# Kernel tuning notes

Hardware: AMD Instinct MI355X
Metric: run time of the kernel (lower is better)

Reference implementation:

```python
import jax, jax.numpy as jnp
import numpy as np

B, N, IN, OUT, H, F = 4, 2048, 128, 64, 4, 64


def setup_inputs() -> dict:
    key = jax.random.key(0)
    ks = jax.random.split(key, 10)
    h = jax.random.normal(ks[0], (B, N, IN), dtype=jnp.float32)
    projection_matrix = jax.random.uniform(ks[1], (B, N, N), dtype=jnp.float32)
    similarity_matrix = jnp.tanh(jax.random.normal(ks[2], (B, N, N), dtype=jnp.float32))
    quadrant_matrix = jax.random.randint(ks[3], (B, N, N, 2), 0, 4)
    # learned params (xavier-ish scaling); stored as (in, out) so x @ W
    W = jax.random.normal(ks[4], (IN, OUT * H), dtype=jnp.float32) * (1.0 / np.sqrt(IN))
    random_projection = jax.random.normal(ks[5], (IN, F), dtype=jnp.float32) * 0.1
    a_q = jax.random.normal(ks[6], (2 * F, OUT), dtype=jnp.float32) * (1.0 / np.sqrt(2 * F))
    a_k = jax.random.normal(ks[7], (2 * F, OUT), dtype=jnp.float32) * (1.0 / np.sqrt(2 * F))
    quadrant_bias = jax.random.normal(ks[8], (4, 4), dtype=jnp.float32) * 0.02
    output_proj = jax.random.normal(ks[9], (OUT * H, OUT), dtype=jnp.float32) * (1.0 / np.sqrt(OUT * H))
    return {
        "h": h,
        "projection_matrix": projection_matrix,
        "similarity_matrix": similarity_matrix,
        "W": W,
        "random_projection": random_projection,
        "a_q": a_q,
        "a_k": a_k,
        "quadrant_bias": quadrant_bias,
        "output_proj": output_proj,
        "quadrant_matrix": quadrant_matrix,
    }


def reference(h, projection_matrix, similarity_matrix, W, random_projection,
              a_q, a_k, quadrant_bias, output_proj, quadrant_matrix):
    # random feature map: phi = [cos(h R), sin(h R)]  -> (B, N, 2F)
    proj = jnp.einsum('bnd,df->bnf', h, random_projection)
    phi = jnp.concatenate([jnp.cos(proj), jnp.sin(proj)], axis=-1)
    Q = phi @ a_q                       # (B, N, OUT)
    K = phi @ a_k                       # (B, N, OUT)
    Wh = (h @ W).reshape(h.shape[0], h.shape[1], H, OUT)  # (B, N, H, OUT)

    scores = jnp.einsum('bio,bjo->bij', Q, K)             # (B, N, N)
    # additive relational biases (shared across heads)
    qb = quadrant_bias[quadrant_matrix[..., 0], quadrant_matrix[..., 1]]  # (B, N, N)
    scores = scores + projection_matrix + similarity_matrix + qb
    attn = jax.nn.softmax(scores[:, None, :, :], axis=-1)  # (B, H, N, N) via broadcast

    # aggregate values per head, then concat heads
    hp = jnp.einsum('bhij,bjhk->bihk', attn, Wh)           # (B, N, H, OUT)
    hp = hp.reshape(h.shape[0], h.shape[1], H * OUT)
    out = hp @ output_proj                                  # (B, N, OUT)
    return jax.nn.elu(out)
```

## Files before the change

### kernel.cpp

```cpp
#include <hip/hip_runtime.h>
#include <math.h>

#define BB   4
#define NN   2048
#define IND  128
#define CDIM 256
#define NIT  16

typedef _Float16 half_t;
typedef _Float16 half4_t __attribute__((ext_vector_type(4)));
typedef _Float16 half8_t __attribute__((ext_vector_type(8)));
typedef float    f32x4   __attribute__((ext_vector_type(4)));

#define SHIFT 16.0f
#define BSCL  6.103515625e-05f
#define BOFF  (-17.5f)

#define NPRE  (BB * NN / 8)
#define NFUSE 2048

__global__ __launch_bounds__(256) void pre_fuse_kernel(
    const float* __restrict__ hg,
    const float* __restrict__ W,
    const float* __restrict__ R,
    const float* __restrict__ aq,
    const float* __restrict__ ak,
    const float* __restrict__ pm,
    const float* __restrict__ sm,
    const int*   __restrict__ qm,
    const float* __restrict__ qbias,
    half_t* __restrict__ Qw,
    half_t* __restrict__ Kw,
    half_t* __restrict__ WhJ,
    unsigned short* __restrict__ bf)
{
    const int tid = threadIdx.x;

    __shared__ float hs[8][IND];
    __shared__ float phis[8][IND];
    __shared__ float qbs[16];

    if (blockIdx.x >= NPRE) {
        if (tid < 16) qbs[tid] = qbias[tid];
        __syncthreads();
        const int nquad  = BB * NN * NN / 4;
        const int stride = NFUSE * 256;
        for (int idx = (blockIdx.x - NPRE) * 256 + tid; idx < nquad; idx += stride) {
            const float4 p  = ((const float4*)pm)[idx];
            const float4 s  = ((const float4*)sm)[idx];
            const int4   qa = ((const int4*)qm)[(size_t)idx * 2];
            const int4   qb = ((const int4*)qm)[(size_t)idx * 2 + 1];
            const float f0 = p.x + s.x + qbs[(qa.x << 2) | qa.y];
            const float f1 = p.y + s.y + qbs[(qa.z << 2) | qa.w];
            const float f2 = p.z + s.z + qbs[(qb.x << 2) | qb.y];
            const float f3 = p.w + s.w + qbs[(qb.z << 2) | qb.w];
            const unsigned u0 = __float2uint_rn(fminf(fmaxf((f0 + 1.5f) * 16384.f, 0.f), 65535.f));
            const unsigned u1 = __float2uint_rn(fminf(fmaxf((f1 + 1.5f) * 16384.f, 0.f), 65535.f));
            const unsigned u2 = __float2uint_rn(fminf(fmaxf((f2 + 1.5f) * 16384.f, 0.f), 65535.f));
            const unsigned u3 = __float2uint_rn(fminf(fmaxf((f3 + 1.5f) * 16384.f, 0.f), 65535.f));
            uint2 o; o.x = u0 | (u1 << 16); o.y = u2 | (u3 << 16);
            ((uint2*)bf)[idx] = o;
        }
        return;
    }

    const int row0 = blockIdx.x * 8;

    {
        const float4* src = (const float4*)(hg + (size_t)row0 * IND);
        ((float4*)&hs[0][0])[tid] = src[tid];
    }
    __syncthreads();

    {
        const int f  = tid & 63;
        const int rr = tid >> 6;
        float p0 = 0.f, p1 = 0.f;
        #pragma unroll 4
        for (int d0 = 0; d0 < IND; d0 += 4) {
            const float r0 = R[(d0 + 0) * 64 + f];
            const float r1 = R[(d0 + 1) * 64 + f];
            const float r2 = R[(d0 + 2) * 64 + f];
            const float r3 = R[(d0 + 3) * 64 + f];
            const float4 ha = *(const float4*)&hs[rr][d0];
            const float4 hb = *(const float4*)&hs[rr + 4][d0];
            p0 += ha.x * r0 + ha.y * r1 + ha.z * r2 + ha.w * r3;
            p1 += hb.x * r0 + hb.y * r1 + hb.z * r2 + hb.w * r3;
        }
        float s, c;
        __sincosf(p0, &s, &c); phis[rr][f]     = c; phis[rr][f + 64]     = s;
        __sincosf(p1, &s, &c); phis[rr + 4][f] = c; phis[rr + 4][f + 64] = s;
    }

    {
        float acc[8];
        #pragma unroll
        for (int r = 0; r < 8; ++r) acc[r] = 0.f;
        #pragma unroll 2
        for (int d0 = 0; d0 < IND; d0 += 4) {
            const float w0 = W[(d0 + 0) * CDIM + tid];
            const float w1 = W[(d0 + 1) * CDIM + tid];
            const float w2 = W[(d0 + 2) * CDIM + tid];
            const float w3 = W[(d0 + 3) * CDIM + tid];
            #pragma unroll
            for (int r = 0; r < 8; ++r) {
                const float4 h4 = *(const float4*)&hs[r][d0];
                acc[r] += h4.x * w0 + h4.y * w1 + h4.z * w2 + h4.w * w3;
            }
        }
        const int b   = row0 >> 11;
        const int j16 = (row0 & (NN - 1)) >> 4;
        const int jr0 = row0 & 8;
        half8_t v;
        #pragma unroll
        for (int r = 0; r < 8; ++r) v[r] = (half_t)acc[r];
        *(half8_t*)(WhJ + (((size_t)b * 128 + j16) * CDIM + tid) * 16 + jr0) = v;
    }
    __syncthreads();

    {
        const int o  = tid & 63;
        const int qk = (tid >> 6) & 1;
        const int rh = tid >> 7;
        const float* A = qk ? ak : aq;
        half_t*    Dst = qk ? Kw : Qw;
        float acc[4] = {0.f, 0.f, 0.f, 0.f};
        #pragma unroll 2
        for (int t0 = 0; t0 < IND; t0 += 4) {
            const float a0 = A[(t0 + 0) * 64 + o];
            const float a1 = A[(t0 + 1) * 64 + o];
            const float a2 = A[(t0 + 2) * 64 + o];
            const float a3 = A[(t0 + 3) * 64 + o];
            #pragma unroll
            for (int r = 0; r < 4; ++r) {
                const float4 ph = *(const float4*)&phis[rh * 4 + r][t0];
                acc[r] += ph.x * a0 + ph.y * a1 + ph.z * a2 + ph.w * a3;
            }
        }
        #pragma unroll
        for (int r = 0; r < 4; ++r)
            Dst[(size_t)(row0 + rh * 4 + r) * 64 + o] = (half_t)acc[r];
    }
}

#define ITERS(IT, KC0, KC1, KN0, KN1, UB, PB)                                   \
  {                                                                             \
       \
    const half_t* wpt = wb + (size_t)(IT) * (8 * CDIM * 16);                    \
    half4_t bwv[16];                                                            \
    _Pragma("unroll")                                                           \
    for (int kk = 0; kk < 8; ++kk) {                                            \
      bwv[2 * kk]     = *(const half4_t*)(wpt + (size_t)kk * (CDIM * 16));      \
      bwv[2 * kk + 1] = *(const half4_t*)(wpt + (size_t)kk * (CDIM * 16) + 256);\
    }                                                                           \
                                     \
    f32x4 s4 = (f32x4){0.f, 0.f, 0.f, 0.f};                                     \
    s4 = __builtin_amdgcn_mfma_f32_16x16x32_f16(KC0, qf0, s4, 0, 0, 0);         \
    s4 = __builtin_amdgcn_mfma_f32_16x16x32_f16(KC1, qf1, s4, 0, 0, 0);         \
    if ((IT) + 1 < NIT) {                                                       \
      const half_t* kp = kbase + (size_t)((IT) + 1) * 128 * 64;                 \
      KN0 = *(const half8_t*)(kp + q * 8);                                      \
      KN1 = *(const half8_t*)(kp + 32 + q * 8);                                 \
    }                                                                           \
    const uint2 uc = UB;                                                        \
    if ((IT) + 2 < NIT)                                                         \
      UB = *(const uint2*)(bfr + (size_t)((IT) + 2) * 128 + cbase);             \
    const float sv0 = s4[0] + fmaf((float)(uc.x & 0xffffu), BSCL, BOFF);        \
    const float sv1 = s4[1] + fmaf((float)(uc.x >> 16),     BSCL, BOFF);        \
    const float sv2 = s4[2] + fmaf((float)(uc.y & 0xffffu), BSCL, BOFF);        \
    const float sv3 = s4[3] + fmaf((float)(uc.y >> 16),     BSCL, BOFF);        \
    const half_t h0 = (half_t)__expf(fminf(sv0, 11.f));                         \
    const half_t h1 = (half_t)__expf(fminf(sv1, 11.f));                         \
    const half_t h2 = (half_t)__expf(fminf(sv2, 11.f));                         \
    const half_t h3 = (half_t)__expf(fminf(sv3, 11.f));                         \
    half4_t aP; aP[0] = h0; aP[1] = h1; aP[2] = h2; aP[3] = h3;                 \
    lacc += (float)h0 + (float)h1 + (float)h2 + (float)h3;                      \
    *(half4_t*)&Pl[PB][w][lane * 4] = aP;                                       \
    asm volatile("s_waitcnt lgkmcnt(0)" ::: "memory");                          \
    __builtin_amdgcn_s_barrier();                                               \
    asm volatile("" ::: "memory");                                              \
                 \
    _Pragma("unroll")                                                           \
    for (int kk = 0; kk < 8; ++kk) {                                            \
      const half4_t pa = *(const half4_t*)&Pl[PB][kk][lane * 4];                \
      acc0 = __builtin_amdgcn_mfma_f32_16x16x16f16(pa, bwv[2 * kk],     acc0, 0, 0, 0); \
      acc1 = __builtin_amdgcn_mfma_f32_16x16x16f16(pa, bwv[2 * kk + 1], acc1, 0, 0, 0); \
    }                                                                           \
  }

__global__ __launch_bounds__(512, 4) void attn4s_kernel(
    const half_t* __restrict__ Qw, const half_t* __restrict__ Kw,
    const half_t* __restrict__ WhJ,
    const unsigned short* __restrict__ bf,
    const float* __restrict__ op,
    float* __restrict__ out)
{
    const int tid  = threadIdx.x;
    const int w    = tid >> 6;
    const int lane = tid & 63;
    const int n    = lane & 15;
    const int q    = lane >> 4;

    const int blk = blockIdx.x;
    const int b   = (blk & 7) >> 1;
    const int i0  = (((blk >> 3) << 1) | (blk & 1)) * 16;

    __shared__ __align__(16) half_t Pl[2][8][256];
    __shared__ __align__(16) float  BufT0[CDIM][20];
    __shared__ float Lp[8][16];

    const half_t* qptr = Qw + ((size_t)(b * NN) + i0 + n) * 64;
    const half8_t qf0 = *(const half8_t*)(qptr + q * 8);
    const half8_t qf1 = *(const half8_t*)(qptr + 32 + q * 8);

    const size_t rowoff = ((size_t)b * NN + i0 + n) * NN;
    const unsigned short* bfr = bf + rowoff;
    const int cbase = w * 16 + q * 4;

    const half_t* kbase = Kw + ((size_t)b * NN + w * 16 + n) * 64;
    const half_t* wb = WhJ + ((size_t)b * 128 * CDIM + (size_t)(w * 32 + n)) * 16 + q * 4;

    uint2 ub0 = *(const uint2*)(bfr + cbase);
    uint2 ub1 = *(const uint2*)(bfr + 128 + cbase);
    half8_t ka0 = *(const half8_t*)(kbase + q * 8);
    half8_t ka1 = *(const half8_t*)(kbase + 32 + q * 8);
    half8_t kb0 = ka0, kb1 = ka1;

    f32x4 acc0 = (f32x4){0.f, 0.f, 0.f, 0.f};
    f32x4 acc1 = (f32x4){0.f, 0.f, 0.f, 0.f};
    float lacc = 0.f;

    for (int it = 0; it < NIT; it += 2) {
        ITERS(it,     ka0, ka1, kb0, kb1, ub0, 0)
        ITERS(it + 1, kb0, kb1, ka0, ka1, ub1, 1)
    }

    lacc += __shfl_xor(lacc, 16);
    lacc += __shfl_xor(lacc, 32);
    if (lane < 16) Lp[w][lane] = lacc;

    *(f32x4*)&BufT0[w * 32 + n][q * 4]      = acc0;
    *(f32x4*)&BufT0[w * 32 + 16 + n][q * 4] = acc1;
    __syncthreads();

    {
        const int r0 = 2 * w, r1 = 2 * w + 1;
        float pacc0 = 0.f, pacc1 = 0.f;
        #pragma unroll 8
        for (int c = 0; c < CDIM; ++c) {
            const float wv = op[c * 64 + lane];
            pacc0 += BufT0[c][r0] * wv;
            pacc1 += BufT0[c][r1] * wv;
        }
        float lt0 = 0.f, lt1 = 0.f;
        #pragma unroll
        for (int gg = 0; gg < 8; ++gg) { lt0 += Lp[gg][r0]; lt1 += Lp[gg][r1]; }
        float x0 = pacc0 / lt0;
        float x1 = pacc1 / lt1;
        x0 = x0 > 0.f ? x0 : (__expf(x0) - 1.f);
        x1 = x1 > 0.f ? x1 : (__expf(x1) - 1.f);
        out[((size_t)b * NN + i0 + r0) * 64 + lane] = x0;
        out[((size_t)b * NN + i0 + r1) * 64 + lane] = x1;
    }
}

#define ITERF(IT, KC0, KC1, KN0, KN1, PB)                                       \
  {                                                                             \
    const half_t* wpt = wb + (size_t)(IT) * (8 * CDIM * 16);                    \
    half4_t bwv[16];                                                            \
    _Pragma("unroll")                                                           \
    for (int kk = 0; kk < 8; ++kk) {                                            \
      bwv[2 * kk]     = *(const half4_t*)(wpt + (size_t)kk * (CDIM * 16));      \
      bwv[2 * kk + 1] = *(const half4_t*)(wpt + (size_t)kk * (CDIM * 16) + 256);\
    }                                                                           \
    f32x4 s4 = (f32x4){0.f, 0.f, 0.f, 0.f};                                     \
    s4 = __builtin_amdgcn_mfma_f32_16x16x32_f16(KC0, qf0, s4, 0, 0, 0);         \
    s4 = __builtin_amdgcn_mfma_f32_16x16x32_f16(KC1, qf1, s4, 0, 0, 0);         \
    if ((IT) + 1 < NIT) {                                                       \
      const half_t* kp = kbase + (size_t)((IT) + 1) * 128 * 64;                 \
      KN0 = *(const half8_t*)(kp + q * 8);                                      \
      KN1 = *(const half8_t*)(kp + 32 + q * 8);                                 \
    }                                                                           \
    const float4 pmC = pmN; const float4 smC = smN;                             \
    const int4 qA = qmN0;  const int4 qB = qmN1;                                \
    if ((IT) + 1 < NIT) {                                                       \
      const int jn = ((IT) + 1) * 128 + cbase;                                  \
      pmN  = *(const float4*)(pmr + jn);                                        \
      smN  = *(const float4*)(smr + jn);                                        \
      qmN0 = *(const int4*)(qmr + (size_t)jn * 2);                              \
      qmN1 = *(const int4*)(qmr + (size_t)jn * 2 + 4);                          \
    }                                                                           \
    const float sv0 = s4[0] + pmC.x + smC.x + qbs[qA.x * 4 + qA.y];             \
    const float sv1 = s4[1] + pmC.y + smC.y + qbs[qA.z * 4 + qA.w];             \
    const float sv2 = s4[2] + pmC.z + smC.z + qbs[qB.x * 4 + qB.y];             \
    const float sv3 = s4[3] + pmC.w + smC.w + qbs[qB.z * 4 + qB.w];             \
    const half_t h0 = (half_t)__expf(fminf(sv0, 11.f));                         \
    const half_t h1 = (half_t)__expf(fminf(sv1, 11.f));                         \
    const half_t h2 = (half_t)__expf(fminf(sv2, 11.f));                         \
    const half_t h3 = (half_t)__expf(fminf(sv3, 11.f));                         \
    half4_t aP; aP[0] = h0; aP[1] = h1; aP[2] = h2; aP[3] = h3;                 \
    lacc += (float)h0 + (float)h1 + (float)h2 + (float)h3;                      \
    *(half4_t*)&Pl[PB][w][lane * 4] = aP;                                       \
    asm volatile("s_waitcnt lgkmcnt(0)" ::: "memory");                          \
    __builtin_amdgcn_s_barrier();                                               \
    asm volatile("" ::: "memory");                                              \
    _Pragma("unroll")                                                           \
    for (int kk = 0; kk < 8; ++kk) {                                            \
      const half4_t pa = *(const half4_t*)&Pl[PB][kk][lane * 4];                \
      acc0 = __builtin_amdgcn_mfma_f32_16x16x16f16(pa, bwv[2 * kk],     acc0, 0, 0, 0); \
      acc1 = __builtin_amdgcn_mfma_f32_16x16x16f16(pa, bwv[2 * kk + 1], acc1, 0, 0, 0); \
    }                                                                           \
  }

__global__ __launch_bounds__(512, 4) void attn4_kernel(
    const half_t* __restrict__ Qw, const half_t* __restrict__ Kw,
    const half_t* __restrict__ WhJ,
    const float* __restrict__ pm, const float* __restrict__ sm,
    const int*   __restrict__ qm, const float* __restrict__ qbias,
    const float* __restrict__ op, float* __restrict__ out)
{
    const int tid  = threadIdx.x;
    const int w    = tid >> 6;
    const int lane = tid & 63;
    const int n    = lane & 15;
    const int q    = lane >> 4;

    const int blk = blockIdx.x;
    const int b   = (blk & 7) >> 1;
    const int i0  = (((blk >> 3) << 1) | (blk & 1)) * 16;

    __shared__ __align__(16) half_t Pl[2][8][256];
    __shared__ __align__(16) float  BufT0[CDIM][20];
    __shared__ float Lp[8][16];
    __shared__ float qbs[16];

    if (tid < 16) qbs[tid] = qbias[tid] - SHIFT;
    __syncthreads();

    const half_t* qptr = Qw + ((size_t)(b * NN) + i0 + n) * 64;
    const half8_t qf0 = *(const half8_t*)(qptr + q * 8);
    const half8_t qf1 = *(const half8_t*)(qptr + 32 + q * 8);

    const size_t rowoff = ((size_t)b * NN + i0 + n) * NN;
    const float* pmr = pm + rowoff;
    const float* smr = sm + rowoff;
    const int*   qmr = qm + rowoff * 2;
    const int cbase = w * 16 + q * 4;

    const half_t* kbase = Kw + ((size_t)b * NN + w * 16 + n) * 64;
    const half_t* wb = WhJ + ((size_t)b * 128 * CDIM + (size_t)(w * 32 + n)) * 16 + q * 4;

    float4 pmN  = *(const float4*)(pmr + cbase);
    float4 smN  = *(const float4*)(smr + cbase);
    int4   qmN0 = *(const int4*)(qmr + cbase * 2);
    int4   qmN1 = *(const int4*)(qmr + cbase * 2 + 4);
    half8_t ka0 = *(const half8_t*)(kbase + q * 8);
    half8_t ka1 = *(const half8_t*)(kbase + 32 + q * 8);
    half8_t kb0 = ka0, kb1 = ka1;

    f32x4 acc0 = (f32x4){0.f, 0.f, 0.f, 0.f};
    f32x4 acc1 = (f32x4){0.f, 0.f, 0.f, 0.f};
    float lacc = 0.f;

    for (int it = 0; it < NIT; it += 2) {
        ITERF(it,     ka0, ka1, kb0, kb1, 0)
        ITERF(it + 1, kb0, kb1, ka0, ka1, 1)
    }

    lacc += __shfl_xor(lacc, 16);
    lacc += __shfl_xor(lacc, 32);
    if (lane < 16) Lp[w][lane] = lacc;

    *(f32x4*)&BufT0[w * 32 + n][q * 4]      = acc0;
    *(f32x4*)&BufT0[w * 32 + 16 + n][q * 4] = acc1;
    __syncthreads();

    {
        const int r0 = 2 * w, r1 = 2 * w + 1;
        float pacc0 = 0.f, pacc1 = 0.f;
        #pragma unroll 8
        for (int c = 0; c < CDIM; ++c) {
            const float wv = op[c * 64 + lane];
            pacc0 += BufT0[c][r0] * wv;
            pacc1 += BufT0[c][r1] * wv;
        }
        float lt0 = 0.f, lt1 = 0.f;
        #pragma unroll
        for (int gg = 0; gg < 8; ++gg) { lt0 += Lp[gg][r0]; lt1 += Lp[gg][r1]; }
        float x0 = pacc0 / lt0;
        float x1 = pacc1 / lt1;
        x0 = x0 > 0.f ? x0 : (__expf(x0) - 1.f);
        x1 = x1 > 0.f ? x1 : (__expf(x1) - 1.f);
        out[((size_t)b * NN + i0 + r0) * 64 + lane] = x0;
        out[((size_t)b * NN + i0 + r1) * 64 + lane] = x1;
    }
}

extern "C" void kernel_launch(void* const* d_in, const int* in_sizes, int n_in,
                              void* d_out, int out_size, void* d_ws, size_t ws_size,
                              hipStream_t stream) {
    (void)in_sizes; (void)n_in; (void)out_size;
    const float* h  = (const float*)d_in[0];
    const float* pm = (const float*)d_in[1];
    const float* sm = (const float*)d_in[2];
    const float* W  = (const float*)d_in[3];
    const float* R  = (const float*)d_in[4];
    const float* aq = (const float*)d_in[5];
    const float* ak = (const float*)d_in[6];
    const float* qb = (const float*)d_in[7];
    const float* op = (const float*)d_in[8];
    const int*   qm = (const int*)d_in[9];
    float* out = (float*)d_out;

    half_t* ws  = (half_t*)d_ws;
    half_t* Qw  = ws;
    half_t* Kw  = ws + (size_t)BB * NN * 64;
    half_t* WhJ = ws + (size_t)BB * NN * 64 * 2;
    unsigned short* bf =
        (unsigned short*)(ws + (size_t)BB * NN * 64 * 2 + (size_t)BB * NN * CDIM);

    const size_t need = ((size_t)BB * NN * 64 * 2 + (size_t)BB * NN * CDIM) * sizeof(half_t)
                      + (size_t)BB * NN * NN * sizeof(unsigned short);

    if (ws_size >= need) {
        pre_fuse_kernel<<<NPRE + NFUSE, 256, 0, stream>>>(
            h, W, R, aq, ak, pm, sm, qm, qb, Qw, Kw, WhJ, bf);
        attn4s_kernel<<<BB * (NN / 16), 512, 0, stream>>>(Qw, Kw, WhJ, bf, op, out);
    } else {
        pre_fuse_kernel<<<NPRE, 256, 0, stream>>>(
            h, W, R, aq, ak, pm, sm, qm, qb, Qw, Kw, WhJ, bf);
        attn4_kernel<<<BB * (NN / 16), 512, 0, stream>>>(Qw, Kw, WhJ, pm, sm, qm, qb, op, out);
    }
}
```

Measured before the change: 391.5 us.

## Retile Wh layout for 8-wide loads, split bias fusion kernel, deepen prefetch

Wh is now stored in a layout where each lane fetches one 8-half vector per k-step, replacing two 4-half loads. The bias pre-fusion (pm+sm+quadrant bias packed into 16-bit) moves out of the precompute kernel into its own software-pipelined kernel, and the attention loop is unrolled by four with bias prefetch four iterations ahead. The aim is fewer, wider global loads and better latency hiding. The cost is an extra kernel launch and higher register pressure.

```diff
diff --git a/kernel.cpp b/kernel.cpp
--- a/kernel.cpp
+++ b/kernel.cpp
@@ -16,55 +16,22 @@
 #define BSCL  6.103515625e-05f
 #define BOFF  (-17.5f)
 
-#define NPRE  (BB * NN / 8)
-#define NFUSE 2048
-
-__global__ __launch_bounds__(256) void pre_fuse_kernel(
+
+__global__ __launch_bounds__(256) void precompute_kernel(
     const float* __restrict__ hg,
     const float* __restrict__ W,
     const float* __restrict__ R,
     const float* __restrict__ aq,
     const float* __restrict__ ak,
-    const float* __restrict__ pm,
-    const float* __restrict__ sm,
-    const int*   __restrict__ qm,
-    const float* __restrict__ qbias,
     half_t* __restrict__ Qw,
     half_t* __restrict__ Kw,
-    half_t* __restrict__ WhJ,
-    unsigned short* __restrict__ bf)
+    half_t* __restrict__ WhJ)
 {
-    const int tid = threadIdx.x;
+    const int tid  = threadIdx.x;
+    const int row0 = blockIdx.x * 8;
 
     __shared__ float hs[8][IND];
     __shared__ float phis[8][IND];
-    __shared__ float qbs[16];
-
-    if (blockIdx.x >= NPRE) {
-        if (tid < 16) qbs[tid] = qbias[tid];
-        __syncthreads();
-        const int nquad  = BB * NN * NN / 4;
-        const int stride = NFUSE * 256;
-        for (int idx = (blockIdx.x - NPRE) * 256 + tid; idx < nquad; idx += stride) {
-            const float4 p  = ((const float4*)pm)[idx];
-            const float4 s  = ((const float4*)sm)[idx];
-            const int4   qa = ((const int4*)qm)[(size_t)idx * 2];
-            const int4   qb = ((const int4*)qm)[(size_t)idx * 2 + 1];
-            const float f0 = p.x + s.x + qbs[(qa.x << 2) | qa.y];
-            const float f1 = p.y + s.y + qbs[(qa.z << 2) | qa.w];
-            const float f2 = p.z + s.z + qbs[(qb.x << 2) | qb.y];
-            const float f3 = p.w + s.w + qbs[(qb.z << 2) | qb.w];
-            const unsigned u0 = __float2uint_rn(fminf(fmaxf((f0 + 1.5f) * 16384.f, 0.f), 65535.f));
-            const unsigned u1 = __float2uint_rn(fminf(fmaxf((f1 + 1.5f) * 16384.f, 0.f), 65535.f));
-            const unsigned u2 = __float2uint_rn(fminf(fmaxf((f2 + 1.5f) * 16384.f, 0.f), 65535.f));
-            const unsigned u3 = __float2uint_rn(fminf(fmaxf((f3 + 1.5f) * 16384.f, 0.f), 65535.f));
-            uint2 o; o.x = u0 | (u1 << 16); o.y = u2 | (u3 << 16);
-            ((uint2*)bf)[idx] = o;
-        }
-        return;
-    }
-
-    const int row0 = blockIdx.x * 8;
 
     {
         const float4* src = (const float4*)(hg + (size_t)row0 * IND);
@@ -110,11 +77,20 @@
         }
         const int b   = row0 >> 11;
         const int j16 = (row0 & (NN - 1)) >> 4;
-        const int jr0 = row0 & 8;
-        half8_t v;
-        #pragma unroll
-        for (int r = 0; r < 8; ++r) v[r] = (half_t)acc[r];
-        *(half8_t*)(WhJ + (((size_t)b * 128 + j16) * CDIM + tid) * 16 + jr0) = v;
+        const int jr0 = row0 & 15;
+        const int fp  = tid >> 5;
+        const int hi  = (tid >> 4) & 1;
+        const int nn2 = tid & 15;
+        half_t* tb = WhJ + ((size_t)(b * 128 + j16)) * 4096
+                   + fp * 512 + nn2 * 32 + hi * 4;
+        #pragma unroll
+        for (int rh = 0; rh < 2; ++rh) {
+            const int qv = (jr0 >> 2) + rh;
+            half4_t v;
+            #pragma unroll
+            for (int k = 0; k < 4; ++k) v[k] = (half_t)acc[rh * 4 + k];
+            *(half4_t*)(tb + qv * 8) = v;
+        }
     }
     __syncthreads();
 
@@ -143,16 +119,54 @@
     }
 }
 
-#define ITERS(IT, KC0, KC1, KN0, KN1, UB, PB)                                   \
+__global__ __launch_bounds__(256, 4) void fuse_bias_kernel(
+    const float* __restrict__ pm, const float* __restrict__ sm,
+    const int*   __restrict__ qm, const float* __restrict__ qbias,
+    unsigned short* __restrict__ bf)
+{
+    __shared__ float qbs[16];
+    if (threadIdx.x < 16) qbs[threadIdx.x] = qbias[threadIdx.x];
+    __syncthreads();
+
+    const int stride = 2048 * 256;
+    int idx = blockIdx.x * 256 + threadIdx.x;
+
+    float4 pA = ((const float4*)pm)[idx];
+    float4 sA = ((const float4*)sm)[idx];
+    int4   qA0 = ((const int4*)qm)[(size_t)idx * 2];
+    int4   qA1 = ((const int4*)qm)[(size_t)idx * 2 + 1];
+
+    #pragma unroll
+    for (int i = 0; i < 8; ++i) {
+        const int nidx = idx + stride;
+        float4 pB, sB; int4 qB0, qB1;
+        if (i + 1 < 8) {
+            pB  = ((const float4*)pm)[nidx];
+            sB  = ((const float4*)sm)[nidx];
+            qB0 = ((const int4*)qm)[(size_t)nidx * 2];
+            qB1 = ((const int4*)qm)[(size_t)nidx * 2 + 1];
+        }
+        const float f0 = pA.x + sA.x + qbs[(qA0.x << 2) | qA0.y];
+        const float f1 = pA.y + sA.y + qbs[(qA0.z << 2) | qA0.w];
+        const float f2 = pA.z + sA.z + qbs[(qA1.x << 2) | qA1.y];
+        const float f3 = pA.w + sA.w + qbs[(qA1.z << 2) | qA1.w];
+        const unsigned u0 = __float2uint_rn(fminf(fmaxf((f0 + 1.5f) * 16384.f, 0.f), 65535.f));
+        const unsigned u1 = __float2uint_rn(fminf(fmaxf((f1 + 1.5f) * 16384.f, 0.f), 65535.f));
+        const unsigned u2 = __float2uint_rn(fminf(fmaxf((f2 + 1.5f) * 16384.f, 0.f), 65535.f));
+        const unsigned u3 = __float2uint_rn(fminf(fmaxf((f3 + 1.5f) * 16384.f, 0.f), 65535.f));
+        uint2 o; o.x = u0 | (u1 << 16); o.y = u2 | (u3 << 16);
+        ((uint2*)bf)[idx] = o;
+        idx = nidx; pA = pB; sA = sB; qA0 = qB0; qA1 = qB1;
+    }
+}
+
+#define ITER7(IT, KC0, KC1, KN0, KN1, UB, PB)                                   \
   {                                                                             \
-       \
-    const half_t* wpt = wb + (size_t)(IT) * (8 * CDIM * 16);                    \
-    half4_t bwv[16];                                                            \
+          \
+    half8_t bwv[8];                                                             \
     _Pragma("unroll")                                                           \
-    for (int kk = 0; kk < 8; ++kk) {                                            \
-      bwv[2 * kk]     = *(const half4_t*)(wpt + (size_t)kk * (CDIM * 16));      \
-      bwv[2 * kk + 1] = *(const half4_t*)(wpt + (size_t)kk * (CDIM * 16) + 256);\
-    }                                                                           \
+    for (int kq = 0; kq < 8; ++kq)                                              \
+      bwv[kq] = *(const half8_t*)(wb + (size_t)((IT) * 8 + kq) * 4096);         \
                                      \
     f32x4 s4 = (f32x4){0.f, 0.f, 0.f, 0.f};                                     \
     s4 = __builtin_amdgcn_mfma_f32_16x16x32_f16(KC0, qf0, s4, 0, 0, 0);         \
@@ -163,8 +177,8 @@
       KN1 = *(const half8_t*)(kp + 32 + q * 8);                                 \
     }                                                                           \
     const uint2 uc = UB;                                                        \
-    if ((IT) + 2 < NIT)                                                         \
-      UB = *(const uint2*)(bfr + (size_t)((IT) + 2) * 128 + cbase);             \
+    if ((IT) + 4 < NIT)                                                         \
+      UB = *(const uint2*)(bfr + (size_t)((IT) + 4) * 128 + cbase);             \
     const float sv0 = s4[0] + fmaf((float)(uc.x & 0xffffu), BSCL, BOFF);        \
     const float sv1 = s4[1] + fmaf((float)(uc.x >> 16),     BSCL, BOFF);        \
     const float sv2 = s4[2] + fmaf((float)(uc.y & 0xffffu), BSCL, BOFF);        \
@@ -181,14 +195,19 @@
     asm volatile("" ::: "memory");                                              \
                  \
     _Pragma("unroll")                                                           \
-    for (int kk = 0; kk < 8; ++kk) {                                            \
-      const half4_t pa = *(const half4_t*)&Pl[PB][kk][lane * 4];                \
-      acc0 = __builtin_amdgcn_mfma_f32_16x16x16f16(pa, bwv[2 * kk],     acc0, 0, 0, 0); \
-      acc1 = __builtin_amdgcn_mfma_f32_16x16x16f16(pa, bwv[2 * kk + 1], acc1, 0, 0, 0); \
+    for (int kq = 0; kq < 8; ++kq) {                                            \
+      const half4_t pa = *(const half4_t*)&Pl[PB][kq][lane * 4];                \
+      half4_t blo, bhi;                                                         \
+      blo[0] = bwv[kq][0]; blo[1] = bwv[kq][1];                                 \
+      blo[2] = bwv[kq][2]; blo[3] = bwv[kq][3];                                 \
+      bhi[0] = bwv[kq][4]; bhi[1] = bwv[kq][5];                                 \
+      bhi[2] = bwv[kq][6]; bhi[3] = bwv[kq][7];                                 \
+      acc0 = __builtin_amdgcn_mfma_f32_16x16x16f16(pa, blo, acc0, 0, 0, 0);     \
+      acc1 = __builtin_amdgcn_mfma_f32_16x16x16f16(pa, bhi, acc1, 0, 0, 0);     \
     }                                                                           \
   }
 
-__global__ __launch_bounds__(512, 4) void attn4s_kernel(
+__global__ __launch_bounds__(512, 4) void attn7_kernel(
     const half_t* __restrict__ Qw, const half_t* __restrict__ Kw,
     const half_t* __restrict__ WhJ,
     const unsigned short* __restrict__ bf,
@@ -218,10 +237,12 @@
     const int cbase = w * 16 + q * 4;
 
     const half_t* kbase = Kw + ((size_t)b * NN + w * 16 + n) * 64;
-    const half_t* wb = WhJ + ((size_t)b * 128 * CDIM + (size_t)(w * 32 + n)) * 16 + q * 4;
+    const half_t* wb = WhJ + (size_t)b * 128 * 4096 + w * 512 + n * 32 + q * 8;
 
     uint2 ub0 = *(const uint2*)(bfr + cbase);
     uint2 ub1 = *(const uint2*)(bfr + 128 + cbase);
+    uint2 ub2 = *(const uint2*)(bfr + 256 + cbase);
+    uint2 ub3 = *(const uint2*)(bfr + 384 + cbase);
     half8_t ka0 = *(const half8_t*)(kbase + q * 8);
     half8_t ka1 = *(const half8_t*)(kbase + 32 + q * 8);
     half8_t kb0 = ka0, kb1 = ka1;
@@ -230,9 +251,11 @@
     f32x4 acc1 = (f32x4){0.f, 0.f, 0.f, 0.f};
     float lacc = 0.f;
 
-    for (int it = 0; it < NIT; it += 2) {
-        ITERS(it,     ka0, ka1, kb0, kb1, ub0, 0)
-        ITERS(it + 1, kb0, kb1, ka0, ka1, ub1, 1)
+    for (int it = 0; it < NIT; it += 4) {
+        ITER7(it,     ka0, ka1, kb0, kb1, ub0, 0)
+        ITER7(it + 1, kb0, kb1, ka0, ka1, ub1, 1)
+        ITER7(it + 2, ka0, ka1, kb0, kb1, ub2, 0)
+        ITER7(it + 3, kb0, kb1, ka0, ka1, ub3, 1)
     }
 
     lacc += __shfl_xor(lacc, 16);
@@ -264,55 +287,7 @@
     }
 }
 
-#define ITERF(IT, KC0, KC1, KN0, KN1, PB)                                       \
-  {                                                                             \
-    const half_t* wpt = wb + (size_t)(IT) * (8 * CDIM * 16);                    \
-    half4_t bwv[16];                                                            \
-    _Pragma("unroll")                                                           \
-    for (int kk = 0; kk < 8; ++kk) {                                            \
-      bwv[2 * kk]     = *(const half4_t*)(wpt + (size_t)kk * (CDIM * 16));      \
-      bwv[2 * kk + 1] = *(const half4_t*)(wpt + (size_t)kk * (CDIM * 16) + 256);\
-    }                                                                           \
-    f32x4 s4 = (f32x4){0.f, 0.f, 0.f, 0.f};                                     \
-    s4 = __builtin_amdgcn_mfma_f32_16x16x32_f16(KC0, qf0, s4, 0, 0, 0);         \
-    s4 = __builtin_amdgcn_mfma_f32_16x16x32_f16(KC1, qf1, s4, 0, 0, 0);         \
-    if ((IT) + 1 < NIT) {                                                       \
-      const half_t* kp = kbase + (size_t)((IT) + 1) * 128 * 64;                 \
-      KN0 = *(const half8_t*)(kp + q * 8);                                      \
-      KN1 = *(const half8_t*)(kp + 32 + q * 8);                                 \
-    }                                                                           \
-    const float4 pmC = pmN; const float4 smC = smN;                             \
-    const int4 qA = qmN0;  const int4 qB = qmN1;                                \
-    if ((IT) + 1 < NIT) {                                                       \
-      const int jn = ((IT) + 1) * 128 + cbase;                                  \
-      pmN  = *(const float4*)(pmr + jn);                                        \
-      smN  = *(const float4*)(smr + jn);                                        \
-      qmN0 = *(const int4*)(qmr + (size_t)jn * 2);                              \
-      qmN1 = *(const int4*)(qmr + (size_t)jn * 2 + 4);                          \
-    }                                                                           \
-    const float sv0 = s4[0] + pmC.x + smC.x + qbs[qA.x * 4 + qA.y];             \
-    const float sv1 = s4[1] + pmC.y + smC.y + qbs[qA.z * 4 + qA.w];             \
-    const float sv2 = s4[2] + pmC.z + smC.z + qbs[qB.x * 4 + qB.y];             \
-    const float sv3 = s4[3] + pmC.w + smC.w + qbs[qB.z * 4 + qB.w];             \
-    const half_t h0 = (half_t)__expf(fminf(sv0, 11.f));                         \
-    const half_t h1 = (half_t)__expf(fminf(sv1, 11.f));                         \
-    const half_t h2 = (half_t)__expf(fminf(sv2, 11.f));                         \
-    const half_t h3 = (half_t)__expf(fminf(sv3, 11.f));                         \
-    half4_t aP; aP[0] = h0; aP[1] = h1; aP[2] = h2; aP[3] = h3;                 \
-    lacc += (float)h0 + (float)h1 + (float)h2 + (float)h3;                      \
-    *(half4_t*)&Pl[PB][w][lane * 4] = aP;                                       \
-    asm volatile("s_waitcnt lgkmcnt(0)" ::: "memory");                          \
-    __builtin_amdgcn_s_barrier();                                               \
-    asm volatile("" ::: "memory");                                              \
-    _Pragma("unroll")                                                           \
-    for (int kk = 0; kk < 8; ++kk) {                                            \
-      const half4_t pa = *(const half4_t*)&Pl[PB][kk][lane * 4];                \
-      acc0 = __builtin_amdgcn_mfma_f32_16x16x16f16(pa, bwv[2 * kk],     acc0, 0, 0, 0); \
-      acc1 = __builtin_amdgcn_mfma_f32_16x16x16f16(pa, bwv[2 * kk + 1], acc1, 0, 0, 0); \
-    }                                                                           \
-  }
-
-__global__ __launch_bounds__(512, 4) void attn4_kernel(
+__global__ __launch_bounds__(512, 4) void attn7f_kernel(
     const half_t* __restrict__ Qw, const half_t* __restrict__ Kw,
     const half_t* __restrict__ WhJ,
     const float* __restrict__ pm, const float* __restrict__ sm,
@@ -348,7 +323,7 @@
     const int cbase = w * 16 + q * 4;
 
     const half_t* kbase = Kw + ((size_t)b * NN + w * 16 + n) * 64;
-    const half_t* wb = WhJ + ((size_t)b * 128 * CDIM + (size_t)(w * 32 + n)) * 16 + q * 4;
+    const half_t* wb = WhJ + (size_t)b * 128 * 4096 + w * 512 + n * 32 + q * 8;
 
     float4 pmN  = *(const float4*)(pmr + cbase);
     float4 smN  = *(const float4*)(smr + cbase);
@@ -356,15 +331,60 @@
     int4   qmN1 = *(const int4*)(qmr + cbase * 2 + 4);
     half8_t ka0 = *(const half8_t*)(kbase + q * 8);
     half8_t ka1 = *(const half8_t*)(kbase + 32 + q * 8);
-    half8_t kb0 = ka0, kb1 = ka1;
 
     f32x4 acc0 = (f32x4){0.f, 0.f, 0.f, 0.f};
     f32x4 acc1 = (f32x4){0.f, 0.f, 0.f, 0.f};
     float lacc = 0.f;
 
-    for (int it = 0; it < NIT; it += 2) {
-        ITERF(it,     ka0, ka1, kb0, kb1, 0)
-        ITERF(it + 1, kb0, kb1, ka0, ka1, 1)
+    for (int it = 0; it < NIT; ++it) {
+        half8_t bwv[8];
+        #pragma unroll
+        for (int kq = 0; kq < 8; ++kq)
+            bwv[kq] = *(const half8_t*)(wb + (size_t)(it * 8 + kq) * 4096);
+
+        f32x4 s4 = (f32x4){0.f, 0.f, 0.f, 0.f};
+        s4 = __builtin_amdgcn_mfma_f32_16x16x32_f16(ka0, qf0, s4, 0, 0, 0);
+        s4 = __builtin_amdgcn_mfma_f32_16x16x32_f16(ka1, qf1, s4, 0, 0, 0);
+        if (it + 1 < NIT) {
+            const half_t* kp = kbase + (size_t)(it + 1) * 128 * 64;
+            ka0 = *(const half8_t*)(kp + q * 8);
+            ka1 = *(const half8_t*)(kp + 32 + q * 8);
+        }
+        const float4 pmC = pmN; const float4 smC = smN;
+        const int4 qA = qmN0;  const int4 qB = qmN1;
+        if (it + 1 < NIT) {
+            const int jn = (it + 1) * 128 + cbase;
+            pmN  = *(const float4*)(pmr + jn);
+            smN  = *(const float4*)(smr + jn);
+            qmN0 = *(const int4*)(qmr + (size_t)jn * 2);
+            qmN1 = *(const int4*)(qmr + (size_t)jn * 2 + 4);
+        }
+        const float sv0 = s4[0] + pmC.x + smC.x + qbs[qA.x * 4 + qA.y];
+        const float sv1 = s4[1] + pmC.y + smC.y + qbs[qA.z * 4 + qA.w];
+        const float sv2 = s4[2] + pmC.z + smC.z + qbs[qB.x * 4 + qB.y];
+        const float sv3 = s4[3] + pmC.w + smC.w + qbs[qB.z * 4 + qB.w];
+        const half_t h0 = (half_t)__expf(fminf(sv0, 11.f));
+        const half_t h1 = (half_t)__expf(fminf(sv1, 11.f));
+        const half_t h2 = (half_t)__expf(fminf(sv2, 11.f));
+        const half_t h3 = (half_t)__expf(fminf(sv3, 11.f));
+        half4_t aP; aP[0] = h0; aP[1] = h1; aP[2] = h2; aP[3] = h3;
+        lacc += (float)h0 + (float)h1 + (float)h2 + (float)h3;
+        const int pb = it & 1;
+        *(half4_t*)&Pl[pb][w][lane * 4] = aP;
+        asm volatile("s_waitcnt lgkmcnt(0)" ::: "memory");
+        __builtin_amdgcn_s_barrier();
+        asm volatile("" ::: "memory");
+        #pragma unroll
+        for (int kq = 0; kq < 8; ++kq) {
+            const half4_t pa = *(const half4_t*)&Pl[pb][kq][lane * 4];
+            half4_t blo, bhi;
+            blo[0] = bwv[kq][0]; blo[1] = bwv[kq][1];
+            blo[2] = bwv[kq][2]; blo[3] = bwv[kq][3];
+            bhi[0] = bwv[kq][4]; bhi[1] = bwv[kq][5];
+            bhi[2] = bwv[kq][6]; bhi[3] = bwv[kq][7];
+            acc0 = __builtin_amdgcn_mfma_f32_16x16x16f16(pa, blo, acc0, 0, 0, 0);
+            acc1 = __builtin_amdgcn_mfma_f32_16x16x16f16(pa, bhi, acc1, 0, 0, 0);
+        }
     }
 
     lacc += __shfl_xor(lacc, 16);
@@ -422,13 +442,11 @@
     const size_t need = ((size_t)BB * NN * 64 * 2 + (size_t)BB * NN * CDIM) * sizeof(half_t)
                       + (size_t)BB * NN * NN * sizeof(unsigned short);
 
+    precompute_kernel<<<BB * NN / 8, 256, 0, stream>>>(h, W, R, aq, ak, Qw, Kw, WhJ);
     if (ws_size >= need) {
-        pre_fuse_kernel<<<NPRE + NFUSE, 256, 0, stream>>>(
-            h, W, R, aq, ak, pm, sm, qm, qb, Qw, Kw, WhJ, bf);
-        attn4s_kernel<<<BB * (NN / 16), 512, 0, stream>>>(Qw, Kw, WhJ, bf, op, out);
+        fuse_bias_kernel<<<2048, 256, 0, stream>>>(pm, sm, qm, qb, bf);
+        attn7_kernel<<<BB * (NN / 16), 512, 0, stream>>>(Qw, Kw, WhJ, bf, op, out);
     } else {
-        pre_fuse_kernel<<<NPRE, 256, 0, stream>>>(
-            h, W, R, aq, ak, pm, sm, qm, qb, Qw, Kw, WhJ, bf);
-        attn4_kernel<<<BB * (NN / 16), 512, 0, stream>>>(Qw, Kw, WhJ, pm, sm, qm, qb, op, out);
+        attn7f_kernel<<<BB * (NN / 16), 512, 0, stream>>>(Qw, Kw, WhJ, pm, sm, qm, qb, op, out);
     }
 }
```

After: 387.6 us. Within noise of the previous version (-1.0%).
